# Kernel optimization log

Hardware: AMD Instinct MI355X
Metric: run time of the kernel (lower is better)

The kernel has to match this reference:

```python
import jax, jax.numpy as jnp
import numpy as np


def setup_inputs() -> dict:
    key = jax.random.key(0)
    ks = jax.random.split(key, 8)
    n_videos, emb_dim = 200000, 128
    n_nodes, k_neigh = 20000, 32
    sc = 1.0 / np.sqrt(emb_dim)
    return {
        "video_embeddings": jax.random.normal(ks[0], (n_videos, emb_dim), jnp.float32),
        "video_nodes": jax.random.randint(ks[1], (n_nodes,), 0, n_videos, jnp.int64 if jax.config.jax_enable_x64 else jnp.int32),
        "neigh_idx": jax.random.randint(ks[2], (n_nodes, k_neigh), 0, n_videos, jnp.int64 if jax.config.jax_enable_x64 else jnp.int32),
        "W1": jax.random.normal(ks[3], (2 * emb_dim, emb_dim), jnp.float32) * sc,
        "b1": jnp.zeros((emb_dim,), jnp.float32),
        "W2": jax.random.normal(ks[4], (emb_dim, emb_dim), jnp.float32) * sc,
        "b2": jnp.zeros((emb_dim,), jnp.float32),
        "W3": jax.random.normal(ks[5], (emb_dim, 1), jnp.float32) * sc,
        "b3": jnp.zeros((1,), jnp.float32),
    }


def reference(video_embeddings, video_nodes, neigh_idx, W1, b1, W2, b2, W3, b3):
    # Ragged per-node loop vectorized as a padded [N, K] neighbor gather.
    neigh_emb = video_embeddings[neigh_idx]          # [N, K, D]
    node_emb = video_embeddings[video_nodes]         # [N, D]
    n, k, d = neigh_emb.shape
    # Attention MLP: cat(neigh, node_repeated) -> relu -> relu -> scalar score
    x = jnp.concatenate([neigh_emb, jnp.broadcast_to(node_emb[:, None, :], (n, k, d))], axis=-1)  # [N, K, 2D]
    h = jax.nn.relu(jnp.einsum("nke,ed->nkd", x, W1) + b1)
    h = jax.nn.relu(jnp.einsum("nke,ed->nkd", h, W2) + b2)
    scores = (jnp.einsum("nkd,do->nko", h, W3) + b3)[..., 0]  # [N, K]
    att = jax.nn.softmax(scores, axis=-1)                      # softmax over neighbors
    # Weighted aggregation: embed_matrix[i] = neigh_emb[i].T @ att[i]
    return jnp.einsum("nkd,nk->nd", neigh_emb, att)
```

## Files before the change

### kernel.cpp

```cpp
#include <hip/hip_runtime.h>
#include <hip/hip_bf16.h>

#define D  128
#define KN 32

typedef __attribute__((ext_vector_type(8))) short bf16x8;
typedef __attribute__((ext_vector_type(4))) float f32x4;

static __device__ __forceinline__ unsigned short f2bf(float f) {
    union { float f; unsigned int u; } v; v.f = f;
    unsigned int u = v.u;
    u += 0x7fff + ((u >> 16) & 1);
    return (unsigned short)(u >> 16);
}
static __device__ __forceinline__ float bf2f(unsigned short h) {
    union { float f; unsigned int u; } v; v.u = ((unsigned int)h) << 16;
    return v.f;
}

__global__ __launch_bounds__(256) void wt_kernel(
    const float* __restrict__ W1, const float* __restrict__ W2,
    unsigned short* __restrict__ W1Tt, unsigned short* __restrict__ W1Tb,
    unsigned short* __restrict__ W2T)
{
    int idx = blockIdx.x * 256 + threadIdx.x;
    if (idx < D * D) {
        int col = idx >> 7, e = idx & 127;
        W1Tt[col * D + e] = f2bf(W1[e * D + col]);
        W1Tb[col * D + e] = f2bf(W1[(D + e) * D + col]);
        W2T [col * D + e] = f2bf(W2[e * D + col]);
    }
}

__global__ __launch_bounds__(256) void p1q_kernel(
    const float* __restrict__ emb, const int* __restrict__ vnodes,
    int NV, int NN, int nvBlocks,
    const unsigned short* __restrict__ W1Tt, const unsigned short* __restrict__ W1Tb,
    const float* __restrict__ b1,
    unsigned short* __restrict__ P1, unsigned short* __restrict__ Q,
    unsigned short* __restrict__ EB)
{
    __shared__ unsigned short sA[128][136];

    const int tid  = threadIdx.x;
    const int lane = tid & 63;
    const int w    = tid >> 6;
    const int m    = lane & 15, q = lane >> 4;

    const bool nv = (int)blockIdx.x < nvBlocks;
    const int  bi = nv ? blockIdx.x : blockIdx.x - nvBlocks;
    const int  M  = nv ? NV : NN;
    const unsigned short* WT = nv ? W1Tt : W1Tb;
    const int r0 = bi * 128;

    int maxRows = M - r0; if (maxRows > 128) maxRows = 128;
    const int maxB = maxRows << 8;

#pragma unroll
    for (int i = 0; i < 16; ++i) {
        int e = tid + 256 * i;
        int row = e >> 5, c4 = (e & 31) << 2;
        int r = r0 + row; if (r > M - 1) r = M - 1;
        int vr = nv ? r : vnodes[r];
        const float4 f = *(const float4*)(emb + (long)vr * D + c4);
        ushort4 h;
        h.x = f2bf(f.x); h.y = f2bf(f.y); h.z = f2bf(f.z); h.w = f2bf(f.w);
        *(ushort4*)(&sA[row][c4]) = h;
    }
    __syncthreads();

    if (nv) {
        char* ebBase = (char*)(EB + (long)r0 * D);
#pragma unroll
        for (int j = 0; j < 8; ++j) {
            int p = j * 4096 + tid * 16;
            if (p < maxB) {
                int row = p >> 8, off = (p & 255) >> 1;
                *(bf16x8*)(ebBase + p) = *(const bf16x8*)(&sA[row][off]);
            }
        }
    }

    bf16x8 Bf[2][4];
#pragma unroll
    for (int nt = 0; nt < 2; ++nt)
#pragma unroll
        for (int kk = 0; kk < 4; ++kk)
            Bf[nt][kk] = *(const bf16x8*)(WT + (32 * w + 16 * nt + m) * D + kk * 32 + q * 8);
    float bv[2];
#pragma unroll
    for (int nt = 0; nt < 2; ++nt) bv[nt] = nv ? 0.f : b1[32 * w + 16 * nt + m];

    f32x4 acc[8][2];
#pragma unroll
    for (int mt = 0; mt < 8; ++mt)
#pragma unroll
        for (int nt = 0; nt < 2; ++nt) acc[mt][nt] = (f32x4){0.f, 0.f, 0.f, 0.f};

#pragma unroll
    for (int kk = 0; kk < 4; ++kk) {
#pragma unroll
        for (int mt = 0; mt < 8; ++mt) {
            bf16x8 a = *(const bf16x8*)(&sA[16 * mt + m][kk * 32 + q * 8]);
            acc[mt][0] = __builtin_amdgcn_mfma_f32_16x16x32_bf16(a, Bf[0][kk], acc[mt][0], 0, 0, 0);
            acc[mt][1] = __builtin_amdgcn_mfma_f32_16x16x32_bf16(a, Bf[1][kk], acc[mt][1], 0, 0, 0);
        }
    }

    __syncthreads();
#pragma unroll
    for (int mt = 0; mt < 8; ++mt)
#pragma unroll
        for (int nt = 0; nt < 2; ++nt) {
            int col = 32 * w + 16 * nt + m;
#pragma unroll
            for (int r = 0; r < 4; ++r)
                sA[16 * mt + 4 * q + r][col] = f2bf(acc[mt][nt][r] + bv[nt]);
        }
    __syncthreads();
    {
        char* dstBase = (char*)((nv ? P1 : Q) + (long)r0 * D);
#pragma unroll
        for (int j = 0; j < 8; ++j) {
            int p = j * 4096 + tid * 16;
            if (p < maxB) {
                int row = p >> 8, off = (p & 255) >> 1;
                *(bf16x8*)(dstBase + p) = *(const bf16x8*)(&sA[row][off]);
            }
        }
    }
}

__global__ __launch_bounds__(256, 2) void agg_kernel(
    const unsigned short* __restrict__ EB, const int* __restrict__ nidx,
    const unsigned short* __restrict__ W2T, const float* __restrict__ b2,
    const float* __restrict__ W3, const float* __restrict__ b3,
    const unsigned short* __restrict__ P1, const unsigned short* __restrict__ Q,
    float* __restrict__ out, int NN)
{
    __shared__ unsigned short sX[128][136];
    __shared__ int   sIdx[128];
    __shared__ float sSp[4][128];
    __shared__ float sAtt[128];

    const int tid  = threadIdx.x;
    const int lane = tid & 63;
    const int w    = tid >> 6;
    const int m    = lane & 15, q = lane >> 4;
    const int row  = tid >> 1, half = tid & 1;

    bf16x8 Bf[2][4];
#pragma unroll
    for (int nt = 0; nt < 2; ++nt)
#pragma unroll
        for (int kk = 0; kk < 4; ++kk)
            Bf[nt][kk] = *(const bf16x8*)(W2T + (32 * w + 16 * nt + m) * D + kk * 32 + q * 8);
    float b2v[2], w3v[2];
#pragma unroll
    for (int nt = 0; nt < 2; ++nt) {
        int col = 32 * w + 16 * nt + m;
        b2v[nt] = b2[col];
        w3v[nt] = W3[col];
    }
    const float b3s = b3[0];

    const int groups = (NN + 3) >> 2;

    int g = blockIdx.x;
    int ni_cur = 0;
    bf16x8 pf[8];
    if (g < groups) {
        int nd = g * 4 + (row >> 5); if (nd > NN - 1) nd = NN - 1;
        ni_cur = nidx[nd * KN + (row & 31)];
#pragma unroll
        for (int j = 0; j < 8; ++j)
            pf[j] = *(const bf16x8*)(P1 + (long)ni_cur * D + half * 64 + j * 8);
    }

    for (; g < groups; g += gridDim.x) {
        const int node0 = g * 4;
        int nd = node0 + (row >> 5); if (nd > NN - 1) nd = NN - 1;

        if (half == 0) sIdx[row] = ni_cur;
        {
            const bf16x8* qq = (const bf16x8*)(Q + (long)nd * D) + half * 8;
#pragma unroll
            for (int j = 0; j < 8; ++j) {
                bf16x8 qv = qq[j], r;
#pragma unroll
                for (int h = 0; h < 8; ++h) {
                    float v = bf2f((unsigned short)pf[j][h]) + bf2f((unsigned short)qv[h]);
                    r[h] = (short)f2bf(v > 0.f ? v : 0.f);
                }
                *(bf16x8*)(&sX[row][half * 64 + j * 8]) = r;
            }
        }

        const int gn = g + gridDim.x;
        const bool more = gn < groups;
        int ni_next = ni_cur;
        if (more) {
            int ndn = gn * 4 + (row >> 5); if (ndn > NN - 1) ndn = NN - 1;
            ni_next = nidx[ndn * KN + (row & 31)];
        }
        __syncthreads();

        bf16x8 gv[8];
#pragma unroll
        for (int j = 0; j < 8; ++j) {
            int k = (lane >> 4) + 4 * j;
            int ik = sIdx[w * KN + k];
            gv[j] = *(const bf16x8*)(EB + (long)ik * D + (lane & 15) * 8);
        }

        if (more) {
#pragma unroll
            for (int j = 0; j < 8; ++j)
                pf[j] = *(const bf16x8*)(P1 + (long)ni_next * D + half * 64 + j * 8);
        }

        f32x4 acc[8][2];
#pragma unroll
        for (int mt = 0; mt < 8; ++mt)
#pragma unroll
            for (int nt = 0; nt < 2; ++nt) acc[mt][nt] = (f32x4){0.f, 0.f, 0.f, 0.f};

#pragma unroll
        for (int kk = 0; kk < 4; ++kk) {
#pragma unroll
            for (int mt = 0; mt < 8; ++mt) {
                bf16x8 a = *(const bf16x8*)(&sX[16 * mt + m][kk * 32 + q * 8]);
                acc[mt][0] = __builtin_amdgcn_mfma_f32_16x16x32_bf16(a, Bf[0][kk], acc[mt][0], 0, 0, 0);
                acc[mt][1] = __builtin_amdgcn_mfma_f32_16x16x32_bf16(a, Bf[1][kk], acc[mt][1], 0, 0, 0);
            }
        }

#pragma unroll
        for (int mt = 0; mt < 8; ++mt) {
            float p[4];
#pragma unroll
            for (int r = 0; r < 4; ++r) {
                float h0 = acc[mt][0][r] + b2v[0]; h0 = h0 > 0.f ? h0 : 0.f;
                float h1 = acc[mt][1][r] + b2v[1]; h1 = h1 > 0.f ? h1 : 0.f;
                p[r] = h0 * w3v[0] + h1 * w3v[1];
            }
#pragma unroll
            for (int off = 8; off >= 1; off >>= 1)
#pragma unroll
                for (int r = 0; r < 4; ++r) p[r] += __shfl_xor(p[r], off, 16);
            if (m == 0) {
#pragma unroll
                for (int r = 0; r < 4; ++r) sSp[w][16 * mt + 4 * q + r] = p[r];
            }
        }
        __syncthreads();

        if (tid < 128) {
            float s = sSp[0][tid] + sSp[1][tid] + sSp[2][tid] + sSp[3][tid] + b3s;
            float mx = s;
#pragma unroll
            for (int off = 16; off >= 1; off >>= 1) mx = fmaxf(mx, __shfl_xor(mx, off, 32));
            float e = __expf(s - mx);
            float sum = e;
#pragma unroll
            for (int off = 16; off >= 1; off >>= 1) sum += __shfl_xor(sum, off, 32);
            sAtt[tid] = e / sum;
        }
        __syncthreads();

        {
            float r[8] = {0.f, 0.f, 0.f, 0.f, 0.f, 0.f, 0.f, 0.f};
#pragma unroll
            for (int j = 0; j < 8; ++j) {
                float a = sAtt[w * KN + (lane >> 4) + 4 * j];
#pragma unroll
                for (int h = 0; h < 8; ++h)
                    r[h] += a * bf2f((unsigned short)gv[j][h]);
            }
#pragma unroll
            for (int h = 0; h < 8; ++h) {
                r[h] += __shfl_xor(r[h], 16);
                r[h] += __shfl_xor(r[h], 32);
            }
            int ndw = node0 + w;
            if (lane < 16 && ndw < NN) {
                float4 o0 = {r[0], r[1], r[2], r[3]};
                float4 o1 = {r[4], r[5], r[6], r[7]};
                *(float4*)(out + (long)ndw * D + lane * 8)     = o0;
                *(float4*)(out + (long)ndw * D + lane * 8 + 4) = o1;
            }
        }
        ni_cur = ni_next;
    }
}

__global__ __launch_bounds__(128) void naive_kernel(
    const float* __restrict__ emb, const int* __restrict__ vnodes,
    const int* __restrict__ nidx,
    const float* __restrict__ W1, const float* __restrict__ b1,
    const float* __restrict__ W2, const float* __restrict__ b2,
    const float* __restrict__ W3, const float* __restrict__ b3,
    float* __restrict__ out)
{
    __shared__ float sE[KN + 1][D];
    __shared__ float sH[KN][D];
    __shared__ float sH2[KN][D];
    __shared__ float sS[KN];
    __shared__ float sA2[KN];
    const int node = blockIdx.x, tid = threadIdx.x;

    for (int r = 0; r < KN + 1; ++r) {
        int vr = (r < KN) ? nidx[node * KN + r] : vnodes[node];
        sE[r][tid] = emb[(long)vr * D + tid];
    }
    __syncthreads();
    for (int k = 0; k < KN; ++k) {
        float s = b1[tid];
        for (int e = 0; e < D; ++e) s += sE[k][e]  * W1[e * D + tid];
        for (int e = 0; e < D; ++e) s += sE[KN][e] * W1[(D + e) * D + tid];
        sH[k][tid] = s > 0.f ? s : 0.f;
    }
    __syncthreads();
    for (int k = 0; k < KN; ++k) {
        float s = b2[tid];
        for (int e = 0; e < D; ++e) s += sH[k][e] * W2[e * D + tid];
        sH2[k][tid] = s > 0.f ? s : 0.f;
    }
    __syncthreads();
    if (tid < KN) {
        float s = b3[0];
        for (int e = 0; e < D; ++e) s += sH2[tid][e] * W3[e];
        sS[tid] = s;
    }
    __syncthreads();
    if (tid == 0) {
        float mx = sS[0];
        for (int k = 1; k < KN; ++k) mx = fmaxf(mx, sS[k]);
        float sum = 0.f;
        for (int k = 0; k < KN; ++k) { sA2[k] = __expf(sS[k] - mx); sum += sA2[k]; }
        for (int k = 0; k < KN; ++k) sA2[k] /= sum;
    }
    __syncthreads();
    float a = 0.f;
    for (int k = 0; k < KN; ++k) a += sA2[k] * sE[k][tid];
    out[(long)node * D + tid] = a;
}

extern "C" void kernel_launch(void* const* d_in, const int* in_sizes, int n_in,
                              void* d_out, int out_size, void* d_ws, size_t ws_size,
                              hipStream_t stream) {
    const float* emb    = (const float*)d_in[0];
    const int*   vnodes = (const int*)d_in[1];
    const int*   nidx   = (const int*)d_in[2];
    const float* W1     = (const float*)d_in[3];
    const float* b1     = (const float*)d_in[4];
    const float* W2     = (const float*)d_in[5];
    const float* b2     = (const float*)d_in[6];
    const float* W3     = (const float*)d_in[7];
    const float* b3     = (const float*)d_in[8];
    float* out = (float*)d_out;

    const int NV = in_sizes[0] / D;
    const int NN = in_sizes[1];

    const size_t p1_elems = (size_t)NV * D;
    const size_t q_elems  = (size_t)NN * D;
    const size_t wt_elems = (size_t)D * D;
    const size_t need = (2 * p1_elems + q_elems + 3 * wt_elems) * sizeof(unsigned short);

    if (ws_size >= need) {
        unsigned short* P1   = (unsigned short*)d_ws;
        unsigned short* Q    = P1 + p1_elems;
        unsigned short* W1Tt = Q + q_elems;
        unsigned short* W1Tb = W1Tt + wt_elems;
        unsigned short* W2T  = W1Tb + wt_elems;
        unsigned short* EB   = W2T + wt_elems;

        const int nvBlocks = (NV + 127) / 128;
        const int qBlocks  = (NN + 127) / 128;

        wt_kernel<<<(D * D + 255) / 256, 256, 0, stream>>>(W1, W2, W1Tt, W1Tb, W2T);
        p1q_kernel<<<nvBlocks + qBlocks, 256, 0, stream>>>(
            emb, vnodes, NV, NN, nvBlocks, W1Tt, W1Tb, b1, P1, Q, EB);
        agg_kernel<<<1024, 256, 0, stream>>>(
            EB, nidx, W2T, b2, W3, b3, P1, Q, out, NN);
    } else {
        naive_kernel<<<NN, D, 0, stream>>>(emb, vnodes, nidx, W1, b1, W2, b2, W3, b3, out);
    }
}
```

Before: 292.5 us.

## Remap agg threads to 16B-column layout, issue EB gather before sync, split MFMA

Each wave now owns one node and each lane loads 8 neighbor rows at a fixed 16-byte column slice, so P1 and EB gathers use the same indices held in registers. That removes the sIdx shared-memory round trip and lets the EB gather be issued before the first barrier. The 8x2 MFMA accumulator tile is split into two halves of 4 to lower register pressure. In exchange, each lane now keeps 8 index registers and does 8 scattered nidx loads per iteration.

```diff
diff --git a/kernel.cpp b/kernel.cpp
--- a/kernel.cpp
+++ b/kernel.cpp
@@ -139,7 +139,6 @@
     float* __restrict__ out, int NN)
 {
     __shared__ unsigned short sX[128][136];
-    __shared__ int   sIdx[128];
     __shared__ float sSp[4][128];
     __shared__ float sAtt[128];
 
@@ -147,7 +146,8 @@
     const int lane = tid & 63;
     const int w    = tid >> 6;
     const int m    = lane & 15, q = lane >> 4;
-    const int row  = tid >> 1, half = tid & 1;
+    const int g4   = q;
+    const int c    = m;
 
     bf16x8 Bf[2][4];
 #pragma unroll
@@ -167,90 +167,90 @@
     const int groups = (NN + 3) >> 2;
 
     int g = blockIdx.x;
-    int ni_cur = 0;
+    int ni[8];
     bf16x8 pf[8];
     if (g < groups) {
-        int nd = g * 4 + (row >> 5); if (nd > NN - 1) nd = NN - 1;
-        ni_cur = nidx[nd * KN + (row & 31)];
-#pragma unroll
-        for (int j = 0; j < 8; ++j)
-            pf[j] = *(const bf16x8*)(P1 + (long)ni_cur * D + half * 64 + j * 8);
+        int nd = g * 4 + w; if (nd > NN - 1) nd = NN - 1;
+#pragma unroll
+        for (int j = 0; j < 8; ++j) {
+            ni[j] = nidx[nd * KN + 4 * j + g4];
+            pf[j] = *(const bf16x8*)(P1 + (long)ni[j] * D + c * 8);
+        }
     }
 
     for (; g < groups; g += gridDim.x) {
         const int node0 = g * 4;
-        int nd = node0 + (row >> 5); if (nd > NN - 1) nd = NN - 1;
-
-        if (half == 0) sIdx[row] = ni_cur;
+        int nd = node0 + w; if (nd > NN - 1) nd = NN - 1;
+
+        bf16x8 gv[8];
+#pragma unroll
+        for (int j = 0; j < 8; ++j)
+            gv[j] = *(const bf16x8*)(EB + (long)ni[j] * D + c * 8);
+
         {
-            const bf16x8* qq = (const bf16x8*)(Q + (long)nd * D) + half * 8;
+            const bf16x8 qv = *(const bf16x8*)(Q + (long)nd * D + c * 8);
 #pragma unroll
             for (int j = 0; j < 8; ++j) {
-                bf16x8 qv = qq[j], r;
+                bf16x8 r;
 #pragma unroll
                 for (int h = 0; h < 8; ++h) {
                     float v = bf2f((unsigned short)pf[j][h]) + bf2f((unsigned short)qv[h]);
                     r[h] = (short)f2bf(v > 0.f ? v : 0.f);
                 }
-                *(bf16x8*)(&sX[row][half * 64 + j * 8]) = r;
+                *(bf16x8*)(&sX[w * 32 + 4 * j + g4][c * 8]) = r;
             }
         }
 
         const int gn = g + gridDim.x;
         const bool more = gn < groups;
-        int ni_next = ni_cur;
+        int nin[8];
         if (more) {
-            int ndn = gn * 4 + (row >> 5); if (ndn > NN - 1) ndn = NN - 1;
-            ni_next = nidx[ndn * KN + (row & 31)];
+            int ndn = gn * 4 + w; if (ndn > NN - 1) ndn = NN - 1;
+#pragma unroll
+            for (int j = 0; j < 8; ++j) nin[j] = nidx[ndn * KN + 4 * j + g4];
         }
         __syncthreads();
 
-        bf16x8 gv[8];
-#pragma unroll
-        for (int j = 0; j < 8; ++j) {
-            int k = (lane >> 4) + 4 * j;
-            int ik = sIdx[w * KN + k];
-            gv[j] = *(const bf16x8*)(EB + (long)ik * D + (lane & 15) * 8);
-        }
-
         if (more) {
 #pragma unroll
             for (int j = 0; j < 8; ++j)
-                pf[j] = *(const bf16x8*)(P1 + (long)ni_next * D + half * 64 + j * 8);
-        }
-
-        f32x4 acc[8][2];
-#pragma unroll
-        for (int mt = 0; mt < 8; ++mt)
-#pragma unroll
-            for (int nt = 0; nt < 2; ++nt) acc[mt][nt] = (f32x4){0.f, 0.f, 0.f, 0.f};
-
-#pragma unroll
-        for (int kk = 0; kk < 4; ++kk) {
-#pragma unroll
-            for (int mt = 0; mt < 8; ++mt) {
-                bf16x8 a = *(const bf16x8*)(&sX[16 * mt + m][kk * 32 + q * 8]);
-                acc[mt][0] = __builtin_amdgcn_mfma_f32_16x16x32_bf16(a, Bf[0][kk], acc[mt][0], 0, 0, 0);
-                acc[mt][1] = __builtin_amdgcn_mfma_f32_16x16x32_bf16(a, Bf[1][kk], acc[mt][1], 0, 0, 0);
-            }
-        }
-
-#pragma unroll
-        for (int mt = 0; mt < 8; ++mt) {
-            float p[4];
-#pragma unroll
-            for (int r = 0; r < 4; ++r) {
-                float h0 = acc[mt][0][r] + b2v[0]; h0 = h0 > 0.f ? h0 : 0.f;
-                float h1 = acc[mt][1][r] + b2v[1]; h1 = h1 > 0.f ? h1 : 0.f;
-                p[r] = h0 * w3v[0] + h1 * w3v[1];
-            }
-#pragma unroll
-            for (int off = 8; off >= 1; off >>= 1)
-#pragma unroll
-                for (int r = 0; r < 4; ++r) p[r] += __shfl_xor(p[r], off, 16);
-            if (m == 0) {
-#pragma unroll
-                for (int r = 0; r < 4; ++r) sSp[w][16 * mt + 4 * q + r] = p[r];
+                pf[j] = *(const bf16x8*)(P1 + (long)nin[j] * D + c * 8);
+        }
+
+#pragma unroll
+        for (int hv = 0; hv < 2; ++hv) {
+            f32x4 acc[4][2];
+#pragma unroll
+            for (int mt = 0; mt < 4; ++mt) {
+                acc[mt][0] = (f32x4){0.f, 0.f, 0.f, 0.f};
+                acc[mt][1] = (f32x4){0.f, 0.f, 0.f, 0.f};
+            }
+#pragma unroll
+            for (int kk = 0; kk < 4; ++kk) {
+#pragma unroll
+                for (int mt = 0; mt < 4; ++mt) {
+                    bf16x8 a = *(const bf16x8*)(&sX[16 * (4 * hv + mt) + m][kk * 32 + q * 8]);
+                    acc[mt][0] = __builtin_amdgcn_mfma_f32_16x16x32_bf16(a, Bf[0][kk], acc[mt][0], 0, 0, 0);
+                    acc[mt][1] = __builtin_amdgcn_mfma_f32_16x16x32_bf16(a, Bf[1][kk], acc[mt][1], 0, 0, 0);
+                }
+            }
+#pragma unroll
+            for (int mt = 0; mt < 4; ++mt) {
+                float p[4];
+#pragma unroll
+                for (int r = 0; r < 4; ++r) {
+                    float h0 = acc[mt][0][r] + b2v[0]; h0 = h0 > 0.f ? h0 : 0.f;
+                    float h1 = acc[mt][1][r] + b2v[1]; h1 = h1 > 0.f ? h1 : 0.f;
+                    p[r] = h0 * w3v[0] + h1 * w3v[1];
+                }
+#pragma unroll
+                for (int off = 8; off >= 1; off >>= 1)
+#pragma unroll
+                    for (int r = 0; r < 4; ++r) p[r] += __shfl_xor(p[r], off, 16);
+                if (m == 0) {
+#pragma unroll
+                    for (int r = 0; r < 4; ++r) sSp[w][16 * (4 * hv + mt) + 4 * q + r] = p[r];
+                }
             }
         }
         __syncthreads();
@@ -269,28 +269,29 @@
         __syncthreads();
 
         {
-            float r[8] = {0.f, 0.f, 0.f, 0.f, 0.f, 0.f, 0.f, 0.f};
+            float r8[8] = {0.f, 0.f, 0.f, 0.f, 0.f, 0.f, 0.f, 0.f};
 #pragma unroll
             for (int j = 0; j < 8; ++j) {
-                float a = sAtt[w * KN + (lane >> 4) + 4 * j];
+                float a = sAtt[w * KN + 4 * j + g4];
 #pragma unroll
                 for (int h = 0; h < 8; ++h)
-                    r[h] += a * bf2f((unsigned short)gv[j][h]);
+                    r8[h] += a * bf2f((unsigned short)gv[j][h]);
             }
 #pragma unroll
             for (int h = 0; h < 8; ++h) {
-                r[h] += __shfl_xor(r[h], 16);
-                r[h] += __shfl_xor(r[h], 32);
+                r8[h] += __shfl_xor(r8[h], 16);
+                r8[h] += __shfl_xor(r8[h], 32);
             }
             int ndw = node0 + w;
-            if (lane < 16 && ndw < NN) {
-                float4 o0 = {r[0], r[1], r[2], r[3]};
-                float4 o1 = {r[4], r[5], r[6], r[7]};
-                *(float4*)(out + (long)ndw * D + lane * 8)     = o0;
-                *(float4*)(out + (long)ndw * D + lane * 8 + 4) = o1;
-            }
-        }
-        ni_cur = ni_next;
+            if (g4 == 0 && ndw < NN) {
+                float4 o0 = {r8[0], r8[1], r8[2], r8[3]};
+                float4 o1 = {r8[4], r8[5], r8[6], r8[7]};
+                *(float4*)(out + (long)ndw * D + c * 8)     = o0;
+                *(float4*)(out + (long)ndw * D + c * 8 + 4) = o1;
+            }
+        }
+#pragma unroll
+        for (int j = 0; j < 8; ++j) ni[j] = nin[j];
     }
 }
 
```

Result: faster. 274.5 us (-6.2%).
